# Optimization experiments

Measured on AMD Instinct MI355X. Metric: run time of the kernel, lower is better.

## Reference

```python
import jax, jax.numpy as jnp
import numpy as np

N = 50000     # nodes
E = 800000    # edges (before self-loops)
DIN = 128     # input feature dim
DH = 16       # per-head hidden dim (layer 1)
H = 8         # heads (layer 1)
DOUT = 64     # output classes (layer 2, heads=1)


def setup_inputs() -> dict:
    key = jax.random.key(0)
    ks = jax.random.split(key, 10)
    def rn(k, shape, scale=0.1):
        return jax.random.normal(k, shape, dtype=jnp.float32) * scale
    x = jax.random.normal(ks[0], (N, DIN), dtype=jnp.float32)
    edge_index = jax.random.randint(ks[1], (2, E), 0, N, dtype=jnp.int64)
    return {
        "x": x,
        "edge_index": edge_index,
        "W1": rn(ks[2], (DIN, H * DH)),
        "a_src1": rn(ks[3], (H, DH)),
        "a_dst1": rn(ks[4], (H, DH)),
        "b1": jnp.zeros((H * DH,), jnp.float32),
        "W2": rn(ks[5], (H * DH, DOUT)),
        "a_src2": rn(ks[6], (1, DOUT)),
        "a_dst2": rn(ks[7], (1, DOUT)),
        "b2": jnp.zeros((DOUT,), jnp.float32),
    }


def gat_conv(x, src, dst, W, a_src, a_dst, b, heads, out_dim):
    """PyG-style GATConv: edge attention + segment softmax over dst + scatter-add."""
    n = x.shape[0]
    h = (x @ W).reshape(n, heads, out_dim)                 # [N, H, D]
    alpha_src = jnp.sum(h * a_src, axis=-1)                # [N, H]
    alpha_dst = jnp.sum(h * a_dst, axis=-1)                # [N, H]
    e = jax.nn.leaky_relu(alpha_src[src] + alpha_dst[dst], 0.2)  # [Etot, H]
    # numerically-stable segment softmax grouped by destination node
    m = jax.ops.segment_max(e, dst, num_segments=n)        # [N, H]
    ex = jnp.exp(e - m[dst])
    s = jax.ops.segment_sum(ex, dst, num_segments=n)       # [N, H]
    alpha = ex / (s[dst] + 1e-16)                          # [Etot, H]
    msg = h[src] * alpha[..., None]                        # [Etot, H, D]
    out = jax.ops.segment_sum(msg, dst, num_segments=n)    # [N, H, D]
    return out.reshape(n, heads * out_dim) + b


def reference(x, W1, a_src1, a_dst1, b1, W2, a_src2, a_dst2, b2, edge_index):
    # eval mode: F.dropout(p=0.6, training=False) is identity
    loop = jnp.arange(N, dtype=edge_index.dtype)
    src = jnp.concatenate([edge_index[0], loop])  # add_self_loops=True (PyG default)
    dst = jnp.concatenate([edge_index[1], loop])
    h = gat_conv(x, src, dst, W1, a_src1, a_dst1, b1, H, DH)
    h = jax.nn.elu(h)
    h = gat_conv(h, src, dst, W2, a_src2, a_dst2, b2, 1, DOUT)
    return (h, jax.nn.log_softmax(h, axis=1))
```

## Files before the change

kernel.cpp:

```cpp
#include <hip/hip_runtime.h>

#define NN 50000
#define EE 800000
#define ET (EE + NN)
#define NCH ((NN + 255) / 256)

typedef unsigned short ushort_t;
using bf16x8 = __attribute__((ext_vector_type(8))) short;
using f32x4  = __attribute__((ext_vector_type(4))) float;

__device__ __forceinline__ float bf2f(ushort_t u) {
    return __uint_as_float(((unsigned int)u) << 16);
}
__device__ __forceinline__ ushort_t f2bf(float f) {
    unsigned int u = __float_as_uint(f);
    u += 0x7fffu + ((u >> 16) & 1u);
    return (ushort_t)(u >> 16);
}
__device__ __forceinline__ float lrelu(float e) {
    return fmaxf(e, 0.f) + 0.2f * fminf(e, 0.f);
}
__device__ __forceinline__ float ldf(const void* p, int i, bool f32) {
    return f32 ? ((const float*)p)[i] : bf2f(((const ushort_t*)p)[i]);
}

__global__ __launch_bounds__(256) void sniff_kernel(const unsigned int* xw, const int* eiw, int* flags) {
    __shared__ int cnt0, cnt1;
    int t = threadIdx.x;
    if (t == 0) { cnt0 = 0; cnt1 = 0; }
    __syncthreads();
    float v = __uint_as_float(xw[t]);
    float a = fabsf(v);
    if ((a > 1e-6f && a < 1e6f) || v == 0.f) atomicAdd(&cnt0, 1);
    if (eiw[2 * t + 1] != 0) atomicAdd(&cnt1, 1);
    __syncthreads();
    if (t == 0) {
        flags[0] = (cnt0 >= 192) ? 1 : 0;
        flags[1] = (cnt1 <= 16) ? 1 : 0;
    }
}

__device__ __forceinline__ void edge_sd(const int* ei, int i, bool i64, int& s, int& d) {
    if (i < EE) {
        if (i64) { s = ei[2 * i]; d = ei[2 * (EE + i)]; }
        else     { s = ei[i];     d = ei[EE + i]; }
    } else {
        s = d = i - EE;
    }
}

__global__ __launch_bounds__(256) void degree_rank_kernel(const int* ei, int* deg8, int* rank, const int* flags) {
    int i = blockIdx.x * 256 + threadIdx.x;
    if (i >= ET) return;
    bool i64 = flags[1] != 0;
    int g = blockIdx.x & 7;
    int s, d;
    edge_sd(ei, i, i64, s, d);
    rank[i] = atomicAdd(&deg8[(size_t)g * NN + d], 1);
}

__global__ __launch_bounds__(256) void scanA_kernel(const int* __restrict__ deg8, int* __restrict__ chunksum) {
    __shared__ int wsum[4];
    int t = threadIdx.x;
    int node = blockIdx.x * 256 + t;
    int v = 0;
    if (node < NN) {
        #pragma unroll
        for (int g = 0; g < 8; ++g) v += deg8[(size_t)g * NN + node];
    }
    int lane = t & 63, wid = t >> 6;
    #pragma unroll
    for (int off = 1; off < 64; off <<= 1) v += __shfl_xor(v, off);
    if (lane == 0) wsum[wid] = v;
    __syncthreads();
    if (t == 0) chunksum[blockIdx.x] = wsum[0] + wsum[1] + wsum[2] + wsum[3];
}

__global__ __launch_bounds__(256) void scanB_kernel(const int* __restrict__ chunksum, int* __restrict__ chunkoff,
                                                    int* __restrict__ rowptr) {
    __shared__ int wsum[4];
    int t = threadIdx.x;
    int lane = t & 63, wid = t >> 6;
    int v = (t < NCH) ? chunksum[t] : 0;
    int x = v;
    #pragma unroll
    for (int off = 1; off < 64; off <<= 1) {
        int y = __shfl_up(x, off);
        if (lane >= off) x += y;
    }
    if (lane == 63) wsum[wid] = x;
    __syncthreads();
    if (t < 4) {
        int s = wsum[t];
        #pragma unroll
        for (int off = 1; off < 4; off <<= 1) {
            int y = __shfl_up(s, off);
            if (t >= off) s += y;
        }
        wsum[t] = s;
    }
    __syncthreads();
    int incl = x + ((wid > 0) ? wsum[wid - 1] : 0);
    if (t < NCH) chunkoff[t] = incl - v;
    if (t == 255) rowptr[NN] = wsum[3];
}

__global__ __launch_bounds__(256) void scanC_kernel(int* __restrict__ deg8, int* __restrict__ rowptr,
                                                    const int* __restrict__ chunkoff) {
    __shared__ int wsum[4];
    int t = threadIdx.x;
    int node = blockIdx.x * 256 + t;
    int dv[8];
    int v = 0;
    if (node < NN) {
        #pragma unroll
        for (int g = 0; g < 8; ++g) {
            dv[g] = deg8[(size_t)g * NN + node];
            v += dv[g];
        }
    }
    int lane = t & 63, wid = t >> 6;
    int x = v;
    #pragma unroll
    for (int off = 1; off < 64; off <<= 1) {
        int y = __shfl_up(x, off);
        if (lane >= off) x += y;
    }
    if (lane == 63) wsum[wid] = x;
    __syncthreads();
    if (t < 4) {
        int s = wsum[t];
        #pragma unroll
        for (int off = 1; off < 4; off <<= 1) {
            int y = __shfl_up(s, off);
            if (t >= off) s += y;
        }
        wsum[t] = s;
    }
    __syncthreads();
    int excl = x - v + ((wid > 0) ? wsum[wid - 1] : 0);
    if (node < NN) {
        int run = chunkoff[blockIdx.x] + excl;
        rowptr[node] = run;
        #pragma unroll
        for (int g = 0; g < 8; ++g) {
            deg8[(size_t)g * NN + node] = run;
            run += dv[g];
        }
    }
}

__global__ __launch_bounds__(256) void fill_kernel(const int* ei, const int* deg8off, const int* rank,
                                                   int* col, const int* flags) {
    int i = blockIdx.x * 256 + threadIdx.x;
    if (i >= ET) return;
    bool i64 = flags[1] != 0;
    int g = blockIdx.x & 7;
    int s, d;
    edge_sd(ei, i, i64, s, d);
    col[deg8off[(size_t)g * NN + d] + rank[i]] = s;
}

__global__ __launch_bounds__(256) void wtprep_kernel(const void* W1v, const void* W2v,
                                                     ushort_t* Wt1, ushort_t* Wt2, const int* flags) {
    bool f32 = flags[0] != 0;
    int i = blockIdx.x * 256 + threadIdx.x;
    if (i < 128 * 128) {
        int k = i >> 7, nc = i & 127;
        ushort_t v = f32 ? f2bf(((const float*)W1v)[i]) : ((const ushort_t*)W1v)[i];
        Wt1[nc * 128 + k] = v;
    }
    int j = i - 128 * 128;
    if (j >= 0 && j < 128 * 64) {
        int k = j >> 6, nc = j & 63;
        ushort_t v = f32 ? f2bf(((const float*)W2v)[j]) : ((const ushort_t*)W2v)[j];
        Wt2[nc * 128 + k] = v;
    }
}

template <bool AEXT, int NCOL, int NH>
__global__ __launch_bounds__(256) void mgemm_kernel(const void* Av, const ushort_t* __restrict__ Wt,
                                                    const void* a_src, const void* a_dst,
                                                    ushort_t* outb, float* asrc, float* adst,
                                                    int n, const int* flags) {
    constexpr int K = 128;
    constexpr int NCT = NCOL / 16;
    bool f32 = flags[0] != 0;
    bool af32 = AEXT && f32;
    int t = threadIdx.x;
    int lane = t & 63, wid = t >> 6;
    int m = lane & 15, quad = lane >> 4;
    int rbase = blockIdx.x * 64 + wid * 16;
    int row = rbase + m;
    bool rok = row < n;

    bf16x8 af[4];
    if (rok) {
        if (!af32) {
            const ushort_t* ap = (const ushort_t*)Av + (size_t)row * K + quad * 8;
            #pragma unroll
            for (int kk = 0; kk < 4; ++kk) af[kk] = *(const bf16x8*)(ap + kk * 32);
        } else {
            const float* ap = (const float*)Av + (size_t)row * K + quad * 8;
            #pragma unroll
            for (int kk = 0; kk < 4; ++kk) {
                float4 q0 = *(const float4*)(ap + kk * 32);
                float4 q1 = *(const float4*)(ap + kk * 32 + 4);
                bf16x8 v;
                v[0] = (short)f2bf(q0.x); v[1] = (short)f2bf(q0.y);
                v[2] = (short)f2bf(q0.z); v[3] = (short)f2bf(q0.w);
                v[4] = (short)f2bf(q1.x); v[5] = (short)f2bf(q1.y);
                v[6] = (short)f2bf(q1.z); v[7] = (short)f2bf(q1.w);
                af[kk] = v;
            }
        }
    } else {
        #pragma unroll
        for (int kk = 0; kk < 4; ++kk) af[kk] = (bf16x8){0, 0, 0, 0, 0, 0, 0, 0};
    }

    f32x4 acc[NCT];
    #pragma unroll
    for (int c = 0; c < NCT; ++c) acc[c] = (f32x4){0.f, 0.f, 0.f, 0.f};

    const ushort_t* wp = Wt + (size_t)m * K + quad * 8;
    #pragma unroll
    for (int c = 0; c < NCT; ++c) {
        const ushort_t* wc = wp + (size_t)c * 16 * K;
        #pragma unroll
        for (int kk = 0; kk < 4; ++kk) {
            bf16x8 bf = *(const bf16x8*)(wc + kk * 32);
            acc[c] = __builtin_amdgcn_mfma_f32_16x16x32_bf16(af[kk], bf, acc[c], 0, 0, 0);
        }
    }

    int orow0 = rbase + quad * 4;
    #pragma unroll
    for (int c = 0; c < NCT; ++c) {
        #pragma unroll
        for (int r = 0; r < 4; ++r) {
            int orow = orow0 + r;
            if (orow < n) outb[(size_t)orow * NCOL + c * 16 + m] = f2bf(acc[c][r]);
        }
    }

    if (NH == 8) {
        #pragma unroll
        for (int c = 0; c < NCT; ++c) {
            float as = ldf(a_src, c * 16 + m, f32);
            float ad = ldf(a_dst, c * 16 + m, f32);
            float ps[4], pd[4];
            #pragma unroll
            for (int r = 0; r < 4; ++r) { ps[r] = acc[c][r] * as; pd[r] = acc[c][r] * ad; }
            #pragma unroll
            for (int stp = 1; stp < 16; stp <<= 1) {
                #pragma unroll
                for (int r = 0; r < 4; ++r) {
                    ps[r] += __shfl_xor(ps[r], stp);
                    pd[r] += __shfl_xor(pd[r], stp);
                }
            }
            if (m == 0) {
                #pragma unroll
                for (int r = 0; r < 4; ++r) {
                    int orow = orow0 + r;
                    if (orow < n) {
                        asrc[(size_t)orow * 8 + c] = ps[r];
                        adst[(size_t)orow * 8 + c] = pd[r];
                    }
                }
            }
        }
    } else {
        float ps[4] = {0.f, 0.f, 0.f, 0.f}, pd[4] = {0.f, 0.f, 0.f, 0.f};
        #pragma unroll
        for (int c = 0; c < NCT; ++c) {
            float as = ldf(a_src, c * 16 + m, f32);
            float ad = ldf(a_dst, c * 16 + m, f32);
            #pragma unroll
            for (int r = 0; r < 4; ++r) {
                ps[r] = fmaf(acc[c][r], as, ps[r]);
                pd[r] = fmaf(acc[c][r], ad, pd[r]);
            }
        }
        #pragma unroll
        for (int stp = 1; stp < 16; stp <<= 1) {
            #pragma unroll
            for (int r = 0; r < 4; ++r) {
                ps[r] += __shfl_xor(ps[r], stp);
                pd[r] += __shfl_xor(pd[r], stp);
            }
        }
        if (m == 0) {
            #pragma unroll
            for (int r = 0; r < 4; ++r) {
                int orow = orow0 + r;
                if (orow < n) { asrc[orow] = ps[r]; adst[orow] = pd[r]; }
            }
        }
    }
}

__global__ __launch_bounds__(256) void agg1_kernel(const int* __restrict__ rowptr, const int* __restrict__ col,
                                                   const ushort_t* __restrict__ h1b,
                                                   const float* __restrict__ asrc, const float* __restrict__ adst,
                                                   const void* b1, ushort_t* __restrict__ hmidb, const int* flags) {
    __shared__ float wle[4][8 * 72];
    __shared__ int loff[4][64];
    bool f32 = flags[0] != 0;
    int lane = threadIdx.x & 63, wid = threadIdx.x >> 6;
    int d = blockIdx.x * 4 + wid;
    if (d >= NN) return;
    int start = rowptr[d], end = rowptr[d + 1];
    int hB = lane >> 3;
    const float4* dp = (const float4*)(adst + (size_t)d * 8);
    float4 ad0 = dp[0], ad1 = dp[1];
    const char* hb = (const char*)h1b + lane * 4;
    float acc0 = 0.f, acc1 = 0.f, ssum = 0.f;
    for (int chunk = start; chunk < end; chunk += 64) {
        int cnt = min(64, end - chunk);
        int c = (chunk + lane < end) ? col[chunk + lane] : 0;
        loff[wid][lane] = c << 8;
        if (lane < cnt) {
            const float4* ap = (const float4*)(asrc + (size_t)c * 8);
            float4 s0 = ap[0], s1 = ap[1];
            wle[wid][0 * 72 + lane] = __expf(lrelu(s0.x + ad0.x));
            wle[wid][1 * 72 + lane] = __expf(lrelu(s0.y + ad0.y));
            wle[wid][2 * 72 + lane] = __expf(lrelu(s0.z + ad0.z));
            wle[wid][3 * 72 + lane] = __expf(lrelu(s0.w + ad0.w));
            wle[wid][4 * 72 + lane] = __expf(lrelu(s1.x + ad1.x));
            wle[wid][5 * 72 + lane] = __expf(lrelu(s1.y + ad1.y));
            wle[wid][6 * 72 + lane] = __expf(lrelu(s1.z + ad1.z));
            wle[wid][7 * 72 + lane] = __expf(lrelu(s1.w + ad1.w));
        }
        #pragma unroll 4
        for (int j = 0; j < cnt; ++j) {
            int off = loff[wid][j];
            float ex = wle[wid][hB * 72 + j];
            unsigned int hv = *(const unsigned int*)(hb + off);
            ssum += ex;
            acc0 = fmaf(ex, __uint_as_float(hv << 16), acc0);
            acc1 = fmaf(ex, __uint_as_float(hv & 0xffff0000u), acc1);
        }
    }
    float inv = 1.f / (ssum + 1e-16f);
    float o0 = fmaf(acc0, inv, ldf(b1, lane * 2, f32));
    float o1 = fmaf(acc1, inv, ldf(b1, lane * 2 + 1, f32));
    o0 = (o0 > 0.f) ? o0 : (__expf(o0) - 1.f);
    o1 = (o1 > 0.f) ? o1 : (__expf(o1) - 1.f);
    unsigned int pk = ((unsigned int)f2bf(o1) << 16) | (unsigned int)f2bf(o0);
    *(unsigned int*)(hmidb + (size_t)d * 128 + lane * 2) = pk;
}

__global__ __launch_bounds__(256) void agg2_kernel(const int* __restrict__ rowptr, const int* __restrict__ col,
                                                   const ushort_t* __restrict__ h2b,
                                                   const float* __restrict__ asrc, const float* __restrict__ adst,
                                                   const void* b2, float* __restrict__ out, const int* flags) {
    __shared__ float wle[4][64];
    __shared__ int loff[4][64];
    bool f32 = flags[0] != 0;
    int lane = threadIdx.x & 63, wid = threadIdx.x >> 6;
    int d = blockIdx.x * 4 + wid;
    if (d >= NN) return;
    int start = rowptr[d], end = rowptr[d + 1];
    float ad = adst[d];
    const char* hb = (const char*)h2b + lane * 2;
    float acc = 0.f, ssum = 0.f;
    for (int chunk = start; chunk < end; chunk += 64) {
        int cnt = min(64, end - chunk);
        int c = (chunk + lane < end) ? col[chunk + lane] : 0;
        loff[wid][lane] = c << 7;
        if (lane < cnt) wle[wid][lane] = __expf(lrelu(asrc[c] + ad));
        #pragma unroll 4
        for (int j = 0; j < cnt; ++j) {
            int off = loff[wid][j];
            float ex = wle[wid][j];
            float hv = bf2f(*(const ushort_t*)(hb + off));
            ssum += ex;
            acc = fmaf(ex, hv, acc);
        }
    }
    float o = acc / (ssum + 1e-16f) + ldf(b2, lane, f32);
    float mm = o;
    #pragma unroll
    for (int off = 1; off < 64; off <<= 1) mm = fmaxf(mm, __shfl_xor(mm, off));
    float texp = __expf(o - mm);
    float ts = texp;
    #pragma unroll
    for (int off = 1; off < 64; off <<= 1) ts += __shfl_xor(ts, off);
    float ls = o - mm - __logf(ts);
    out[(size_t)d * 64 + lane] = o;
    out[(size_t)NN * 64 + (size_t)d * 64 + lane] = ls;
}

extern "C" void kernel_launch(void* const* d_in, const int* in_sizes, int n_in,
                              void* d_out, int out_size, void* d_ws, size_t ws_size,
                              hipStream_t stream) {
    const void* x   = d_in[0];
    const int*  ei  = (const int*)d_in[1];
    const void* W1  = d_in[2];
    const void* as1 = d_in[3];
    const void* ad1 = d_in[4];
    const void* b1  = d_in[5];
    const void* W2  = d_in[6];
    const void* as2 = d_in[7];
    const void* ad2 = d_in[8];
    const void* b2  = d_in[9];
    float* out = (float*)d_out;

    char* w = (char*)d_ws;
    auto alloc = [&](size_t bytes) {
        void* p = (void*)w;
        w += (bytes + 255) & ~(size_t)255;
        return p;
    };
    int* flags    = (int*)alloc(256);
    int* deg8     = (int*)alloc((size_t)8 * NN * 4);
    int* rowptr   = (int*)alloc((size_t)(NN + 1) * 4);
    int* chunksum = (int*)alloc((size_t)NCH * 4);
    int* chunkoff = (int*)alloc((size_t)NCH * 4);
    int* rank     = (int*)alloc((size_t)ET * 4);
    int* colx     = (int*)alloc((size_t)ET * 4);
    ushort_t* Wt1 = (ushort_t*)alloc((size_t)128 * 128 * 2);
    ushort_t* Wt2 = (ushort_t*)alloc((size_t)64 * 128 * 2);
    ushort_t* h1b = (ushort_t*)alloc((size_t)NN * 128 * 2);
    float* asrc1  = (float*)alloc((size_t)NN * 8 * 4);
    float* adst1  = (float*)alloc((size_t)NN * 8 * 4);
    ushort_t* hmidb = (ushort_t*)alloc((size_t)NN * 128 * 2);
    ushort_t* h2b = (ushort_t*)alloc((size_t)NN * 64 * 2);
    float* asrc2  = (float*)alloc((size_t)NN * 4);
    float* adst2  = (float*)alloc((size_t)NN * 4);

    sniff_kernel<<<1, 256, 0, stream>>>((const unsigned int*)x, ei, flags);

    hipMemsetAsync(deg8, 0, (size_t)8 * NN * 4, stream);
    degree_rank_kernel<<<(ET + 255) / 256, 256, 0, stream>>>(ei, deg8, rank, flags);
    scanA_kernel<<<NCH, 256, 0, stream>>>(deg8, chunksum);
    scanB_kernel<<<1, 256, 0, stream>>>(chunksum, chunkoff, rowptr);
    scanC_kernel<<<NCH, 256, 0, stream>>>(deg8, rowptr, chunkoff);
    fill_kernel<<<(ET + 255) / 256, 256, 0, stream>>>(ei, deg8, rank, colx, flags);
    wtprep_kernel<<<(128 * 128 + 128 * 64 + 255) / 256, 256, 0, stream>>>(W1, W2, Wt1, Wt2, flags);

    int gblocks = (NN + 63) / 64;
    mgemm_kernel<true, 128, 8><<<gblocks, 256, 0, stream>>>(x, Wt1, as1, ad1, h1b, asrc1, adst1, NN, flags);
    agg1_kernel<<<(NN + 3) / 4, 256, 0, stream>>>(rowptr, colx, h1b, asrc1, adst1, b1, hmidb, flags);

    mgemm_kernel<false, 64, 1><<<gblocks, 256, 0, stream>>>((const void*)hmidb, Wt2, as2, ad2, h2b, asrc2, adst2, NN, flags);
    agg2_kernel<<<(NN + 3) / 4, 256, 0, stream>>>(rowptr, colx, h2b, asrc2, adst2, b2, out, flags);
}
```

Baseline: 265.2 us.

## Fuse CSR build launches with decoupled-lookback scan and inline dtype sniffing

The separate sniff kernel and flags buffer are removed. Each kernel now detects the dtype per wave with a ballot. The degree count and weight transpose are merged into one prep launch. The three-pass scan becomes a single-pass decoupled-lookback scan that runs in the same launch as the first GEMM, and the fill step now takes positions with atomics instead of storing and rereading a rank array. Together these cut the kernel launch count and the global traffic for the rank buffer. The cost is a spin-wait scan whose correctness relies on earlier blocks being scheduled first, and edge order within a row becomes nondeterministic.

```diff
diff --git a/kernel.cpp b/kernel.cpp
--- a/kernel.cpp
+++ b/kernel.cpp
@@ -4,6 +4,9 @@
 #define EE 800000
 #define ET (EE + NN)
 #define NCH ((NN + 255) / 256)
+#define DEGB ((ET + 255) / 256)
+#define WPB ((128 * 128 + 128 * 64 + 255) / 256)
+#define GEMB ((NN + 63) / 64)
 
 typedef unsigned short ushort_t;
 using bf16x8 = __attribute__((ext_vector_type(8))) short;
@@ -24,20 +27,18 @@
     return f32 ? ((const float*)p)[i] : bf2f(((const ushort_t*)p)[i]);
 }
 
-__global__ __launch_bounds__(256) void sniff_kernel(const unsigned int* xw, const int* eiw, int* flags) {
-    __shared__ int cnt0, cnt1;
-    int t = threadIdx.x;
-    if (t == 0) { cnt0 = 0; cnt1 = 0; }
-    __syncthreads();
-    float v = __uint_as_float(xw[t]);
+__device__ __forceinline__ bool sniff_f32(const unsigned int* __restrict__ xw) {
+    int lane = threadIdx.x & 63;
+    float v = __uint_as_float(xw[lane]);
     float a = fabsf(v);
-    if ((a > 1e-6f && a < 1e6f) || v == 0.f) atomicAdd(&cnt0, 1);
-    if (eiw[2 * t + 1] != 0) atomicAdd(&cnt1, 1);
-    __syncthreads();
-    if (t == 0) {
-        flags[0] = (cnt0 >= 192) ? 1 : 0;
-        flags[1] = (cnt1 <= 16) ? 1 : 0;
-    }
+    bool ok = (a > 1e-6f && a < 1e6f) || v == 0.f;
+    unsigned long long m = __ballot(ok);
+    return __popcll(m) >= 48;
+}
+__device__ __forceinline__ bool sniff_i64(const int* __restrict__ eiw) {
+    int lane = threadIdx.x & 63;
+    unsigned long long m = __ballot(eiw[2 * lane + 1] != 0);
+    return __popcll(m) <= 4;
 }
 
 __device__ __forceinline__ void edge_sd(const int* ei, int i, bool i64, int& s, int& d) {
@@ -48,40 +49,59 @@
         s = d = i - EE;
     }
 }
-
-__global__ __launch_bounds__(256) void degree_rank_kernel(const int* ei, int* deg8, int* rank, const int* flags) {
-    int i = blockIdx.x * 256 + threadIdx.x;
-    if (i >= ET) return;
-    bool i64 = flags[1] != 0;
-    int g = blockIdx.x & 7;
-    int s, d;
-    edge_sd(ei, i, i64, s, d);
-    rank[i] = atomicAdd(&deg8[(size_t)g * NN + d], 1);
-}
-
-__global__ __launch_bounds__(256) void scanA_kernel(const int* __restrict__ deg8, int* __restrict__ chunksum) {
+__device__ __forceinline__ int edge_d(const int* ei, int i, bool i64) {
+    if (i < EE) return i64 ? ei[2 * (EE + i)] : ei[EE + i];
+    return i - EE;
+}
+
+__global__ __launch_bounds__(256) void prep_kernel(const int* __restrict__ ei, int* __restrict__ deg8,
+                                                   const unsigned int* __restrict__ xw,
+                                                   const void* W1v, const void* W2v,
+                                                   ushort_t* __restrict__ Wt1, ushort_t* __restrict__ Wt2) {
+    int b = blockIdx.x;
+    if (b < DEGB) {
+        bool i64 = sniff_i64(ei);
+        int i = b * 256 + threadIdx.x;
+        if (i >= ET) return;
+        int g = b & 7;
+        int d = edge_d(ei, i, i64);
+        atomicAdd(&deg8[(size_t)g * NN + d], 1);
+    } else {
+        bool f32 = sniff_f32(xw);
+        int i = (b - DEGB) * 256 + threadIdx.x;
+        if (i < 128 * 128) {
+            int k = i >> 7, nc = i & 127;
+            ushort_t v = f32 ? f2bf(((const float*)W1v)[i]) : ((const ushort_t*)W1v)[i];
+            Wt1[nc * 128 + k] = v;
+        }
+        int j = i - 128 * 128;
+        if (j >= 0 && j < 128 * 64) {
+            int k = j >> 6, nc = j & 63;
+            ushort_t v = f32 ? f2bf(((const float*)W2v)[j]) : ((const ushort_t*)W2v)[j];
+            Wt2[nc * 128 + k] = v;
+        }
+    }
+}
+
+#define FLG_A (1ull << 62)
+#define FLG_P (2ull << 62)
+
+__device__ void scan_body(int b, int* __restrict__ deg8, int* __restrict__ rowptr,
+                          unsigned long long* __restrict__ state) {
     __shared__ int wsum[4];
+    __shared__ int bpref;
     int t = threadIdx.x;
-    int node = blockIdx.x * 256 + t;
+    int node = b * 256 + t;
+    int lane = t & 63, wid = t >> 6;
+    int dv[8];
     int v = 0;
     if (node < NN) {
         #pragma unroll
-        for (int g = 0; g < 8; ++g) v += deg8[(size_t)g * NN + node];
-    }
-    int lane = t & 63, wid = t >> 6;
-    #pragma unroll
-    for (int off = 1; off < 64; off <<= 1) v += __shfl_xor(v, off);
-    if (lane == 0) wsum[wid] = v;
-    __syncthreads();
-    if (t == 0) chunksum[blockIdx.x] = wsum[0] + wsum[1] + wsum[2] + wsum[3];
-}
-
-__global__ __launch_bounds__(256) void scanB_kernel(const int* __restrict__ chunksum, int* __restrict__ chunkoff,
-                                                    int* __restrict__ rowptr) {
-    __shared__ int wsum[4];
-    int t = threadIdx.x;
-    int lane = t & 63, wid = t >> 6;
-    int v = (t < NCH) ? chunksum[t] : 0;
+        for (int g = 0; g < 8; ++g) {
+            dv[g] = deg8[(size_t)g * NN + node];
+            v += dv[g];
+        }
+    }
     int x = v;
     #pragma unroll
     for (int off = 1; off < 64; off <<= 1) {
@@ -100,47 +120,30 @@
         wsum[t] = s;
     }
     __syncthreads();
-    int incl = x + ((wid > 0) ? wsum[wid - 1] : 0);
-    if (t < NCH) chunkoff[t] = incl - v;
-    if (t == 255) rowptr[NN] = wsum[3];
-}
-
-__global__ __launch_bounds__(256) void scanC_kernel(int* __restrict__ deg8, int* __restrict__ rowptr,
-                                                    const int* __restrict__ chunkoff) {
-    __shared__ int wsum[4];
-    int t = threadIdx.x;
-    int node = blockIdx.x * 256 + t;
-    int dv[8];
-    int v = 0;
-    if (node < NN) {
-        #pragma unroll
-        for (int g = 0; g < 8; ++g) {
-            dv[g] = deg8[(size_t)g * NN + node];
-            v += dv[g];
-        }
-    }
-    int lane = t & 63, wid = t >> 6;
-    int x = v;
-    #pragma unroll
-    for (int off = 1; off < 64; off <<= 1) {
-        int y = __shfl_up(x, off);
-        if (lane >= off) x += y;
-    }
-    if (lane == 63) wsum[wid] = x;
-    __syncthreads();
-    if (t < 4) {
-        int s = wsum[t];
-        #pragma unroll
-        for (int off = 1; off < 4; off <<= 1) {
-            int y = __shfl_up(s, off);
-            if (t >= off) s += y;
-        }
-        wsum[t] = s;
+    int total = wsum[3];
+    if (t == 0) {
+        int prefix = 0;
+        if (b == 0) {
+            atomicExch(&state[0], FLG_P | (unsigned long long)(unsigned)total);
+        } else {
+            atomicExch(&state[b], FLG_A | (unsigned long long)(unsigned)total);
+            int j = b - 1;
+            while (true) {
+                unsigned long long sv = atomicAdd(&state[j], 0ull);
+                unsigned long long f = sv >> 62;
+                if (f == 0) { __builtin_amdgcn_s_sleep(2); continue; }
+                prefix += (int)(unsigned)(sv & 0xffffffffull);
+                if (f == 2) break;
+                --j;
+            }
+            atomicExch(&state[b], FLG_P | (unsigned long long)(unsigned)(prefix + total));
+        }
+        bpref = prefix;
     }
     __syncthreads();
     int excl = x - v + ((wid > 0) ? wsum[wid - 1] : 0);
     if (node < NN) {
-        int run = chunkoff[blockIdx.x] + excl;
+        int run = bpref + excl;
         rowptr[node] = run;
         #pragma unroll
         for (int g = 0; g < 8; ++g) {
@@ -148,49 +151,21 @@
             run += dv[g];
         }
     }
-}
-
-__global__ __launch_bounds__(256) void fill_kernel(const int* ei, const int* deg8off, const int* rank,
-                                                   int* col, const int* flags) {
-    int i = blockIdx.x * 256 + threadIdx.x;
-    if (i >= ET) return;
-    bool i64 = flags[1] != 0;
-    int g = blockIdx.x & 7;
-    int s, d;
-    edge_sd(ei, i, i64, s, d);
-    col[deg8off[(size_t)g * NN + d] + rank[i]] = s;
-}
-
-__global__ __launch_bounds__(256) void wtprep_kernel(const void* W1v, const void* W2v,
-                                                     ushort_t* Wt1, ushort_t* Wt2, const int* flags) {
-    bool f32 = flags[0] != 0;
-    int i = blockIdx.x * 256 + threadIdx.x;
-    if (i < 128 * 128) {
-        int k = i >> 7, nc = i & 127;
-        ushort_t v = f32 ? f2bf(((const float*)W1v)[i]) : ((const ushort_t*)W1v)[i];
-        Wt1[nc * 128 + k] = v;
-    }
-    int j = i - 128 * 128;
-    if (j >= 0 && j < 128 * 64) {
-        int k = j >> 6, nc = j & 63;
-        ushort_t v = f32 ? f2bf(((const float*)W2v)[j]) : ((const ushort_t*)W2v)[j];
-        Wt2[nc * 128 + k] = v;
-    }
+    if (b == NCH - 1 && t == 255) rowptr[NN] = bpref + total;
 }
 
 template <bool AEXT, int NCOL, int NH>
-__global__ __launch_bounds__(256) void mgemm_kernel(const void* Av, const ushort_t* __restrict__ Wt,
-                                                    const void* a_src, const void* a_dst,
-                                                    ushort_t* outb, float* asrc, float* adst,
-                                                    int n, const int* flags) {
+__device__ __forceinline__ void mgemm_body(int bid, const void* Av, const ushort_t* __restrict__ Wt,
+                                           const void* a_src, const void* a_dst,
+                                           ushort_t* __restrict__ outb, float* __restrict__ asrc,
+                                           float* __restrict__ adst, int n, bool f32) {
     constexpr int K = 128;
     constexpr int NCT = NCOL / 16;
-    bool f32 = flags[0] != 0;
     bool af32 = AEXT && f32;
     int t = threadIdx.x;
     int lane = t & 63, wid = t >> 6;
     int m = lane & 15, quad = lane >> 4;
-    int rbase = blockIdx.x * 64 + wid * 16;
+    int rbase = bid * 64 + wid * 16;
     int row = rbase + m;
     bool rok = row < n;
 
@@ -301,13 +276,48 @@
     }
 }
 
-__global__ __launch_bounds__(256) void agg1_kernel(const int* __restrict__ rowptr, const int* __restrict__ col,
+__global__ __launch_bounds__(256) void scan_mgemm1_kernel(int* __restrict__ deg8, int* __restrict__ rowptr,
+                                                          unsigned long long* __restrict__ state,
+                                                          const void* xv, const ushort_t* __restrict__ Wt1,
+                                                          const void* as1, const void* ad1,
+                                                          ushort_t* __restrict__ h1b,
+                                                          float* __restrict__ asrc1, float* __restrict__ adst1) {
+    if (blockIdx.x < NCH) {
+        scan_body(blockIdx.x, deg8, rowptr, state);
+        return;
+    }
+    bool f32 = sniff_f32((const unsigned int*)xv);
+    mgemm_body<true, 128, 8>(blockIdx.x - NCH, xv, Wt1, as1, ad1, h1b, asrc1, adst1, NN, f32);
+}
+
+__global__ __launch_bounds__(256) void mgemm2_kernel(const void* Av, const ushort_t* __restrict__ Wt,
+                                                     const void* a_src, const void* a_dst,
+                                                     ushort_t* __restrict__ outb, float* __restrict__ asrc,
+                                                     float* __restrict__ adst, const unsigned int* __restrict__ xw) {
+    bool f32 = sniff_f32(xw);
+    mgemm_body<false, 64, 1>(blockIdx.x, Av, Wt, a_src, a_dst, outb, asrc, adst, NN, f32);
+}
+
+__global__ __launch_bounds__(256) void fill_kernel(const int* __restrict__ ei, int* __restrict__ deg8,
+                                                   int* __restrict__ col) {
+    bool i64 = sniff_i64(ei);
+    int i = blockIdx.x * 256 + threadIdx.x;
+    if (i >= ET) return;
+    int g = blockIdx.x & 7;
+    int s, d;
+    edge_sd(ei, i, i64, s, d);
+    int pos = atomicAdd(&deg8[(size_t)g * NN + d], 1);
+    col[pos] = s;
+}
+
+__global__ __launch_bounds__(256) void agg1_kernel(const unsigned int* __restrict__ xw,
+                                                   const int* __restrict__ rowptr, const int* __restrict__ col,
                                                    const ushort_t* __restrict__ h1b,
                                                    const float* __restrict__ asrc, const float* __restrict__ adst,
-                                                   const void* b1, ushort_t* __restrict__ hmidb, const int* flags) {
+                                                   const void* b1, ushort_t* __restrict__ hmidb) {
     __shared__ float wle[4][8 * 72];
     __shared__ int loff[4][64];
-    bool f32 = flags[0] != 0;
+    bool f32 = sniff_f32(xw);
     int lane = threadIdx.x & 63, wid = threadIdx.x >> 6;
     int d = blockIdx.x * 4 + wid;
     if (d >= NN) return;
@@ -352,13 +362,14 @@
     *(unsigned int*)(hmidb + (size_t)d * 128 + lane * 2) = pk;
 }
 
-__global__ __launch_bounds__(256) void agg2_kernel(const int* __restrict__ rowptr, const int* __restrict__ col,
+__global__ __launch_bounds__(256) void agg2_kernel(const unsigned int* __restrict__ xw,
+                                                   const int* __restrict__ rowptr, const int* __restrict__ col,
                                                    const ushort_t* __restrict__ h2b,
                                                    const float* __restrict__ asrc, const float* __restrict__ adst,
-                                                   const void* b2, float* __restrict__ out, const int* flags) {
+                                                   const void* b2, float* __restrict__ out) {
     __shared__ float wle[4][64];
     __shared__ int loff[4][64];
-    bool f32 = flags[0] != 0;
+    bool f32 = sniff_f32(xw);
     int lane = threadIdx.x & 63, wid = threadIdx.x >> 6;
     int d = blockIdx.x * 4 + wid;
     if (d >= NN) return;
@@ -414,12 +425,9 @@
         w += (bytes + 255) & ~(size_t)255;
         return p;
     };
-    int* flags    = (int*)alloc(256);
-    int* deg8     = (int*)alloc((size_t)8 * NN * 4);
+    int* deg8     = (int*)alloc((size_t)8 * NN * 4 + 4096);
+    unsigned long long* state = (unsigned long long*)((char*)deg8 + (size_t)8 * NN * 4);
     int* rowptr   = (int*)alloc((size_t)(NN + 1) * 4);
-    int* chunksum = (int*)alloc((size_t)NCH * 4);
-    int* chunkoff = (int*)alloc((size_t)NCH * 4);
-    int* rank     = (int*)alloc((size_t)ET * 4);
     int* colx     = (int*)alloc((size_t)ET * 4);
     ushort_t* Wt1 = (ushort_t*)alloc((size_t)128 * 128 * 2);
     ushort_t* Wt2 = (ushort_t*)alloc((size_t)64 * 128 * 2);
@@ -431,20 +439,16 @@
     float* asrc2  = (float*)alloc((size_t)NN * 4);
     float* adst2  = (float*)alloc((size_t)NN * 4);
 
-    sniff_kernel<<<1, 256, 0, stream>>>((const unsigned int*)x, ei, flags);
-
-    hipMemsetAsync(deg8, 0, (size_t)8 * NN * 4, stream);
-    degree_rank_kernel<<<(ET + 255) / 256, 256, 0, stream>>>(ei, deg8, rank, flags);
-    scanA_kernel<<<NCH, 256, 0, stream>>>(deg8, chunksum);
-    scanB_kernel<<<1, 256, 0, stream>>>(chunksum, chunkoff, rowptr);
-    scanC_kernel<<<NCH, 256, 0, stream>>>(deg8, rowptr, chunkoff);
-    fill_kernel<<<(ET + 255) / 256, 256, 0, stream>>>(ei, deg8, rank, colx, flags);
-    wtprep_kernel<<<(128 * 128 + 128 * 64 + 255) / 256, 256, 0, stream>>>(W1, W2, Wt1, Wt2, flags);
-
-    int gblocks = (NN + 63) / 64;
-    mgemm_kernel<true, 128, 8><<<gblocks, 256, 0, stream>>>(x, Wt1, as1, ad1, h1b, asrc1, adst1, NN, flags);
-    agg1_kernel<<<(NN + 3) / 4, 256, 0, stream>>>(rowptr, colx, h1b, asrc1, adst1, b1, hmidb, flags);
-
-    mgemm_kernel<false, 64, 1><<<gblocks, 256, 0, stream>>>((const void*)hmidb, Wt2, as2, ad2, h2b, asrc2, adst2, NN, flags);
-    agg2_kernel<<<(NN + 3) / 4, 256, 0, stream>>>(rowptr, colx, h2b, asrc2, adst2, b2, out, flags);
-}
+    hipMemsetAsync(deg8, 0, (size_t)8 * NN * 4 + (size_t)NCH * 8, stream);
+
+    prep_kernel<<<DEGB + WPB, 256, 0, stream>>>(ei, deg8, (const unsigned int*)x, W1, W2, Wt1, Wt2);
+    scan_mgemm1_kernel<<<NCH + GEMB, 256, 0, stream>>>(deg8, rowptr, state, x, Wt1, as1, ad1,
+                                                       h1b, asrc1, adst1);
+    fill_kernel<<<DEGB, 256, 0, stream>>>(ei, deg8, colx);
+    agg1_kernel<<<(NN + 3) / 4, 256, 0, stream>>>((const unsigned int*)x, rowptr, colx, h1b,
+                                                  asrc1, adst1, b1, hmidb);
+    mgemm2_kernel<<<GEMB, 256, 0, stream>>>((const void*)hmidb, Wt2, as2, ad2, h2b, asrc2, adst2,
+                                            (const unsigned int*)x);
+    agg2_kernel<<<(NN + 3) / 4, 256, 0, stream>>>((const unsigned int*)x, rowptr, colx, h2b,
+                                                  asrc2, adst2, b2, out);
+}
```

After: 291.6 us. 1.1x slower.
